# Optimization experiments

Hardware: AMD Instinct MI355X
Metric: run time of the kernel (lower is better)

## Reference

```python
import jax, jax.numpy as jnp
import numpy as np

B, T, F, H, OUT = 128, 512, 1, 512, 1


def setup_inputs() -> dict:
    key = jax.random.key(0)
    ks = jax.random.split(key, 12)
    s1 = 1.0 / np.sqrt(H)  # torch LSTMCell/Linear default init scale
    u = lambda k, shape, s: jax.random.uniform(k, shape, jnp.float32, -s, s)
    return {
        "x": jax.random.normal(ks[0], (B, T), jnp.float32),
        "W_ih1": u(ks[1], (4 * H, F), s1),
        "W_hh1": u(ks[2], (4 * H, H), s1),
        "b_ih1": u(ks[3], (4 * H,), s1),
        "b_hh1": u(ks[4], (4 * H,), s1),
        "W_ih2": u(ks[5], (4 * H, H), s1),
        "W_hh2": u(ks[6], (4 * H, H), s1),
        "b_ih2": u(ks[7], (4 * H,), s1),
        "b_hh2": u(ks[8], (4 * H,), s1),
        "W_out": u(ks[9], (OUT, H), s1),
        "b_out": u(ks[10], (OUT,), s1),
        "future": 32,
    }


def _lstm_cell(x_t, h, c, W_ih, W_hh, b_ih, b_hh):
    # gates: [B, 4H]; torch LSTMCell gate order: i, f, g, o
    gates = x_t @ W_ih.T + b_ih + h @ W_hh.T + b_hh
    i, f, g, o = jnp.split(gates, 4, axis=-1)
    c_new = jax.nn.sigmoid(f) * c + jax.nn.sigmoid(i) * jnp.tanh(g)
    h_new = jax.nn.sigmoid(o) * jnp.tanh(c_new)
    return h_new, c_new


def reference(x, W_ih1, W_hh1, b_ih1, b_hh1, W_ih2, W_hh2, b_ih2, b_hh2,
              W_out, b_out, future):
    bsz = x.shape[0]
    hid = W_hh1.shape[1]
    zeros = jnp.zeros((bsz, hid), x.dtype)

    def run_cells(x_t, h1, c1, h2, c2):
        h1, c1 = _lstm_cell(x_t, h1, c1, W_ih1, W_hh1, b_ih1, b_hh1)
        h2, c2 = _lstm_cell(h1, h2, c2, W_ih2, W_hh2, b_ih2, b_hh2)
        out = h2 @ W_out.T + b_out  # [B, 1]
        return h1, c1, h2, c2, out

    def step(carry, x_t):
        h1, c1, h2, c2 = carry
        h1, c1, h2, c2, out = run_cells(x_t, h1, c1, h2, c2)
        return (h1, c1, h2, c2), out

    xs = jnp.swapaxes(x, 0, 1)[..., None]  # [T, B, 1]
    carry, outs = jax.lax.scan(step, (zeros, zeros, zeros, zeros), xs)

    if future > 0:
        def fstep(carry, _):
            h1, c1, h2, c2, out = carry
            h1, c1, h2, c2, out = run_cells(out, h1, c1, h2, c2)
            return (h1, c1, h2, c2, out), out

        fcarry = (*carry, outs[-1])
        _, fouts = jax.lax.scan(fstep, fcarry, None, length=future)
        outs = jnp.concatenate([outs, fouts], axis=0)  # [T+future, B, 1]

    # stack(dim=1).squeeze(2) -> [B, T+future]
    return jnp.swapaxes(outs, 0, 1)[..., 0]
```

## Files before the change

kernel.cpp:

```cpp
#include <hip/hip_runtime.h>
#include <cstdint>

#define Hdim 512
#define Bdim 128
#define Tdim 512
#define FUT  32
#define TT   (Tdim + FUT)
#define NB1  64
#define NB2  128
#define NBO  2
#define NBLK (NB1 + NB2 + NBO)
#define RD   8
#define FSTR 32
#define F2B  64
#define FOB  200

typedef _Float16 f16;
typedef f16   half8 __attribute__((ext_vector_type(8)));
typedef float f32x4 __attribute__((ext_vector_type(4)));
typedef unsigned long long ull;

#define AW1_OFF 0
#define AW2_OFF (AW1_OFF + 1048576)
#define B1P_OFF (AW2_OFF + 2097152)
#define B2P_OFF (B1P_OFF + 2048)
#define WX1_OFF (B2P_OFF + 2048)
#define XT_OFF  (WX1_OFF + 2048)
#define H1P_OFF (XT_OFF + 65536)
#define H2P_OFF (H1P_OFF + 524288)
#define ARR_OFF (H2P_OFF + 524288)
#define WS_FLOATS (ARR_OFF + 8192)

__device__ __forceinline__ float sigm(float v) { return 1.0f / (1.0f + __expf(-v)); }
__device__ __forceinline__ float tanh_fast(float v) {
    v = fminf(fmaxf(v, -20.0f), 20.0f);
    float e = __expf(2.0f * v);
    return (e - 1.0f) / (e + 1.0f);
}

__device__ __forceinline__ unsigned cohloadu(const unsigned* p) {
    return __hip_atomic_load(p, __ATOMIC_RELAXED, __HIP_MEMORY_SCOPE_AGENT);
}
__device__ __forceinline__ ull cohload64(const ull* p) {
    return __hip_atomic_load(p, __ATOMIC_RELAXED, __HIP_MEMORY_SCOPE_AGENT);
}
__device__ __forceinline__ void cohstore64(ull* p, ull v) {
    __hip_atomic_store(p, v, __ATOMIC_RELAXED, __HIP_MEMORY_SCOPE_AGENT);
}

union HB { ull u[2]; half8 h; };
__device__ __forceinline__ half8 fragload(const half8* p) {
    const ull* q = (const ull*)p;
    HB t; t.u[0] = cohload64(q); t.u[1] = cohload64(q + 1);
    return t.h;
}

__global__ void lstm_prep(const float* __restrict__ x,
                          const float* __restrict__ W_ih1, const float* __restrict__ W_hh1,
                          const float* __restrict__ b_ih1, const float* __restrict__ b_hh1,
                          const float* __restrict__ W_ih2, const float* __restrict__ W_hh2,
                          const float* __restrict__ b_ih2, const float* __restrict__ b_hh2,
                          float* __restrict__ ws) {
    int i = blockIdx.x * blockDim.x + threadIdx.x;
    f16* aw1 = (f16*)(ws + AW1_OFF);
    f16* aw2 = (f16*)(ws + AW2_OFF);

    if (i < 131072) {
        int mt = i >> 10, rest = i & 1023, ks = rest >> 6, lane = rest & 63;
        int m = mt * 16 + (lane & 15);
        int u = m >> 2, g = m & 3;
        int kbase = ks * 32 + (lane >> 4) * 8;
        size_t ohi = ((((size_t)mt * 16 + ks) * 2 + 0) * 64 + lane) * 8;
        size_t olo = ((((size_t)mt * 16 + ks) * 2 + 1) * 64 + lane) * 8;
        #pragma unroll
        for (int j = 0; j < 8; ++j) {
            float wv = W_hh1[(size_t)(g * Hdim + u) * Hdim + kbase + j];
            f16 hi = (f16)wv;
            f16 lo = (f16)(wv - (float)hi);
            aw1[ohi + j] = hi; aw1[olo + j] = lo;
        }
    }
    if (i >= 131072 && i < 393216) {
        int i2 = i - 131072;
        int mt = i2 >> 11, rest = i2 & 2047, ks = rest >> 6, lane = rest & 63;
        int m = mt * 16 + (lane & 15);
        int u = m >> 2, g = m & 3;
        int kbase = ks * 32 + (lane >> 4) * 8;
        size_t ohi = ((((size_t)mt * 32 + ks) * 2 + 0) * 64 + lane) * 8;
        size_t olo = ((((size_t)mt * 32 + ks) * 2 + 1) * 64 + lane) * 8;
        #pragma unroll
        for (int j = 0; j < 8; ++j) {
            int k = kbase + j;
            float wv = (k < Hdim) ? W_ih2[(size_t)(g * Hdim + u) * Hdim + k]
                                  : W_hh2[(size_t)(g * Hdim + u) * Hdim + (k - Hdim)];
            f16 hi = (f16)wv;
            f16 lo = (f16)(wv - (float)hi);
            aw2[ohi + j] = hi; aw2[olo + j] = lo;
        }
    }
    if (i < Hdim) {
        float4 bb1 = { b_ih1[i] + b_hh1[i],               b_ih1[Hdim+i] + b_hh1[Hdim+i],
                       b_ih1[2*Hdim+i] + b_hh1[2*Hdim+i], b_ih1[3*Hdim+i] + b_hh1[3*Hdim+i] };
        float4 bb2 = { b_ih2[i] + b_hh2[i],               b_ih2[Hdim+i] + b_hh2[Hdim+i],
                       b_ih2[2*Hdim+i] + b_hh2[2*Hdim+i], b_ih2[3*Hdim+i] + b_hh2[3*Hdim+i] };
        float4 wx  = { W_ih1[i], W_ih1[Hdim+i], W_ih1[2*Hdim+i], W_ih1[3*Hdim+i] };
        ((float4*)(ws + B1P_OFF))[i] = bb1;
        ((float4*)(ws + B2P_OFF))[i] = bb2;
        ((float4*)(ws + WX1_OFF))[i] = wx;
    }
    if (i < Tdim * Bdim) {
        int t = i >> 7, b = i & 127;
        ws[XT_OFF + i] = x[b * Tdim + t];
    }
    if (i < 262144) {
        ((ull*)(ws + H1P_OFF))[i] = 0;
        ((ull*)(ws + H2P_OFF))[i] = 0;
    }
    if (i < 8192) ((unsigned*)(ws + ARR_OFF))[i] = 0u;
}

__global__ __launch_bounds__(256, 1) void lstm_main(float* ws,
                                                    const float* __restrict__ Wout,
                                                    const float* __restrict__ bout,
                                                    float* __restrict__ out) {
    const int tid  = threadIdx.x, bid = blockIdx.x;
    const int w    = tid >> 6;
    const int lane = tid & 63;
    const int quad = lane >> 4;
    const int col  = lane & 15;
    const bool is1  = (bid < NB1);
    const bool is2  = (bid >= NB1) && (bid < NB1 + NB2);
    const bool isout = (bid >= NB1 + NB2);

    __shared__ f16   awlds[65536];
    __shared__ float wout_lds[Hdim];
    __shared__ float psum[4][64];
    __shared__ float xflds[64];
    __shared__ float qpart[4][64];
    __shared__ ull   hstg[512];

    unsigned* flg = (unsigned*)(ws + ARR_OFF);
    unsigned short* stg = (unsigned short*)hstg;
    const float* xT = ws + XT_OFF;
    const float bout0 = bout[0];

    const int bid1 = is1 ? (bid & 31) : 0;
    const int gid  = is2 ? (bid - NB1) : 0;
    const int ug   = gid & 63;
    const int gA   = is1 ? (bid >> 5) : (is2 ? (gid >> 6) : (bid - NB1 - NB2));
    const int ntw  = gA * 4 + w;
    const int ks1  = bid1 >> 1, qp0 = (bid1 & 1) * 2;
    const int ks2  = ug >> 2,  qg  = ug & 3;

    auto wait3 = [&](unsigned T1, unsigned T2) {
        if (tid < 64) {
            for (;;) {
                unsigned v1 = (lane < 32) ? cohloadu(flg + (gA*32 + lane) * FSTR) : 0xFFFFFFFFu;
                unsigned v2 = cohloadu(flg + (F2B + gA*64 + lane) * FSTR);
                if (__all(v1 >= T1 && v2 >= T2)) break;
                __builtin_amdgcn_s_sleep(4);
            }
        }
        asm volatile("" ::: "memory");
        __syncthreads();
    };
    auto wait1o = [&](unsigned T1, unsigned To) {
        if (tid < 64) {
            for (;;) {
                unsigned v1 = (lane < 32) ? cohloadu(flg + (gA*32 + lane) * FSTR)  : 0xFFFFFFFFu;
                unsigned vo = (lane == 0) ? cohloadu(flg + (FOB + gA) * FSTR)      : 0xFFFFFFFFu;
                if (__all(v1 >= T1 && vo >= To)) break;
                __builtin_amdgcn_s_sleep(4);
            }
        }
        asm volatile("" ::: "memory");
        __syncthreads();
    };
    auto wait2f = [&](unsigned T2) {
        if (tid < 64) {
            for (;;) {
                unsigned v2 = cohloadu(flg + (F2B + gA*64 + lane) * FSTR);
                if (__all(v2 >= T2)) break;
                __builtin_amdgcn_s_sleep(4);
            }
        }
        asm volatile("" ::: "memory");
        __syncthreads();
    };
    auto post = [&](unsigned* slot, unsigned val) {
        __syncthreads();
        if (tid == 0)
            __hip_atomic_store(slot, val, __ATOMIC_RELAXED, __HIP_MEMORY_SCOPE_AGENT);
    };

    auto h1pf = [&](int par, int spl) {
        return (const half8*)((const unsigned short*)(ws + H1P_OFF) + (size_t)(par*2+spl) * 65536); };
    auto h2pf = [&](int par, int spl) {
        return (const half8*)((const unsigned short*)(ws + H2P_OFF) + (size_t)(par*2+spl) * 65536); };
    auto h1ull = [&](int par, int spl) {
        return (ull*)(ws + H1P_OFF) + (size_t)(par*2+spl) * 16384; };
    auto h2ull = [&](int par, int spl) {
        return (ull*)(ws + H2P_OFF) + (size_t)(par*2+spl) * 16384; };

    if (is1) {
        half8* d = (half8*)awlds;
        const half8* s = (const half8*)(ws + AW1_OFF) + (size_t)bid1 * 8192;
        for (int i = tid; i < 8192; i += 256) d[i] = s[i];
    } else if (is2) {
        half8* d = (half8*)awlds;
        const half8* s = (const half8*)(ws + AW2_OFF) + (size_t)ug * 8192;
        for (int i = tid; i < 8192; i += 256) d[i] = s[i];
    }
    wout_lds[tid]       = Wout[tid];
    wout_lds[256 + tid] = Wout[256 + tid];
    __syncthreads();
    const half8* aw8 = (const half8*)awlds;

    const int bcol = ntw * 16 + col;
    int   u_[4];  float4 b1v[4], wxv[4];  float c1s[4];
    int   u2_[2]; float4 b2v[2];          float c2s[2];
    if (is1) {
        #pragma unroll
        for (int mt = 0; mt < 4; ++mt) {
            u_[mt]  = bid1 * 16 + mt * 4 + quad;
            b1v[mt] = ((const float4*)(ws + B1P_OFF))[u_[mt]];
            wxv[mt] = ((const float4*)(ws + WX1_OFF))[u_[mt]];
            c1s[mt] = 0.0f;
        }
    } else if (is2) {
        #pragma unroll
        for (int mt = 0; mt < 2; ++mt) {
            u2_[mt] = ug * 8 + mt * 4 + quad;
            b2v[mt] = ((const float4*)(ws + B2P_OFF))[u2_[mt]];
            c2s[mt] = 0.0f;
        }
    }

    auto stage1 = [&](int mt, float hv) {
        f16 hhi = (f16)hv;
        f16 hlo = (f16)(hv - (float)hhi);
        int mq = mt*4 + quad, qp = mq >> 3, jj = mq & 7;
        int hi = ((w*2 + qp)*16 + col)*8 + jj;
        stg[hi]        = __builtin_bit_cast(unsigned short, hhi);
        stg[1024 + hi] = __builtin_bit_cast(unsigned short, hlo);
    };
    auto store1 = [&](int dpar) {
        __syncthreads();
        #pragma unroll
        for (int k = 0; k < 2; ++k) {
            int f = k * 256 + tid;
            int spl = f >> 8, r = f & 255;
            int ntl = r >> 6, rr = r & 63;
            int qp = rr >> 5, r2 = rr & 31, colp = r2 >> 1, pos = r2 & 1;
            cohstore64(h1ull(dpar, spl)
                       + (((gA*4 + ntl)*16 + ks1)*64 + (qp0 + qp)*16 + colp)*2 + pos,
                       hstg[f]);
        }
    };

    auto gemm1 = [&](int spar, int dpar, float xv) {
        f32x4 acc[4] = {};
        const half8* fh = h1pf(spar, 0);
        const half8* fl = h1pf(spar, 1);
        half8 rh[8], rl[8];
        #pragma unroll
        for (int ks = 0; ks < 8; ++ks) {
            rh[ks] = fragload(fh + (ntw*16+ks)*64 + lane);
            rl[ks] = fragload(fl + (ntw*16+ks)*64 + lane);
        }
        #pragma unroll
        for (int ks = 0; ks < 16; ++ks) {
            half8 b0h = rh[ks&7], b0l = rl[ks&7];
            if (ks < 8) {
                int kp = ks + 8;
                rh[ks&7] = fragload(fh + (ntw*16+kp)*64 + lane);
                rl[ks&7] = fragload(fl + (ntw*16+kp)*64 + lane);
            }
            #pragma unroll
            for (int mt = 0; mt < 4; ++mt) {
                half8 ah = aw8[((mt*16 + ks)*2 + 0)*64 + lane];
                half8 al = aw8[((mt*16 + ks)*2 + 1)*64 + lane];
                acc[mt] = __builtin_amdgcn_mfma_f32_16x16x32_f16(ah, b0h, acc[mt], 0, 0, 0);
                acc[mt] = __builtin_amdgcn_mfma_f32_16x16x32_f16(al, b0h, acc[mt], 0, 0, 0);
                acc[mt] = __builtin_amdgcn_mfma_f32_16x16x32_f16(ah, b0l, acc[mt], 0, 0, 0);
            }
        }
        #pragma unroll
        for (int mt = 0; mt < 4; ++mt) {
            f32x4 g = acc[mt];
            float pi = g[0] + b1v[mt].x + wxv[mt].x * xv;
            float pf = g[1] + b1v[mt].y + wxv[mt].y * xv;
            float pg = g[2] + b1v[mt].z + wxv[mt].z * xv;
            float po = g[3] + b1v[mt].w + wxv[mt].w * xv;
            float c = fmaf(sigm(pf), c1s[mt], sigm(pi) * tanh_fast(pg));
            c1s[mt] = c;
            stage1(mt, sigm(po) * tanh_fast(c));
        }
        store1(dpar);
    };

    auto g2_step = [&](int s) {
        int cpar = s & 7, ppar = (s - 1) & 7;
        const half8* fh = h1pf(cpar, 0);
        const half8* fl = h1pf(cpar, 1);
        const half8* gh = h2pf(ppar, 0);
        const half8* gl = h2pf(ppar, 1);

        wait1o((unsigned)(s + 1), (s >= RD) ? (unsigned)(s - (RD - 1)) : 0u);
        half8 rh[8], rl[8];
        #pragma unroll
        for (int ks = 0; ks < 8; ++ks) {
            rh[ks] = fragload(fh + (ntw*16+ks)*64 + lane);
            rl[ks] = fragload(fl + (ntw*16+ks)*64 + lane);
        }
        wait2f((unsigned)s);

        f32x4 acc[2] = {};
        #pragma unroll
        for (int ks = 0; ks < 32; ++ks) {
            half8 b0h = rh[ks&7], b0l = rl[ks&7];
            if (ks < 24) {
                int kp = ks + 8;
                const half8* sh = (kp < 16) ? fh : gh;
                const half8* sl = (kp < 16) ? fl : gl;
                int kq = (kp < 16) ? kp : kp - 16;
                rh[ks&7] = fragload(sh + (ntw*16+kq)*64 + lane);
                rl[ks&7] = fragload(sl + (ntw*16+kq)*64 + lane);
            }
            #pragma unroll
            for (int mt = 0; mt < 2; ++mt) {
                half8 ah = aw8[((mt*32 + ks)*2 + 0)*64 + lane];
                half8 al = aw8[((mt*32 + ks)*2 + 1)*64 + lane];
                acc[mt] = __builtin_amdgcn_mfma_f32_16x16x32_f16(ah, b0h, acc[mt], 0, 0, 0);
                acc[mt] = __builtin_amdgcn_mfma_f32_16x16x32_f16(al, b0h, acc[mt], 0, 0, 0);
                acc[mt] = __builtin_amdgcn_mfma_f32_16x16x32_f16(ah, b0l, acc[mt], 0, 0, 0);
            }
        }
        #pragma unroll
        for (int mt = 0; mt < 2; ++mt) {
            f32x4 g = acc[mt];
            float pi = g[0] + b2v[mt].x;
            float pf = g[1] + b2v[mt].y;
            float pg = g[2] + b2v[mt].z;
            float po = g[3] + b2v[mt].w;
            float c = fmaf(sigm(pf), c2s[mt], sigm(pi) * tanh_fast(pg));
            c2s[mt] = c;
            float hv = sigm(po) * tanh_fast(c);
            f16 hhi = (f16)hv;
            f16 hlo = (f16)(hv - (float)hhi);
            int idx = ((w*16 + col)*8 + (mt*4 + quad));
            stg[idx]       = __builtin_bit_cast(unsigned short, hhi);
            stg[512 + idx] = __builtin_bit_cast(unsigned short, hlo);
        }
        __syncthreads();
        {
            int f = tid;
            int spl = f >> 7, r = f & 127;
            int ntl = r >> 5, colp = (r >> 1) & 15, pos = r & 1;
            int nt = gA * 4 + ntl;
            cohstore64(h2ull(cpar, spl) + ((nt*16 + ks2)*64 + qg*16 + colp)*2 + pos, hstg[f]);
        }
        post(&flg[(F2B + gA*64 + ug) * FSTR], (unsigned)(s + 1));
    };

    if (is1) {
        #pragma unroll
        for (int mt = 0; mt < 4; ++mt) {
            float xv = xT[bcol];
            float pi = b1v[mt].x + wxv[mt].x * xv;
            float pg = b1v[mt].z + wxv[mt].z * xv;
            float po = b1v[mt].w + wxv[mt].w * xv;
            float c = sigm(pi) * tanh_fast(pg);
            c1s[mt] = c;
            stage1(mt, sigm(po) * tanh_fast(c));
        }
        store1(0);
        post(&flg[(gA*32 + bid1) * FSTR], 1u);

        for (int t = 0; t <= Tdim - 2; ++t) {
            wait3((unsigned)(t + 1), (t >= RD - 1) ? (unsigned)(t - (RD - 2)) : 0u);
            gemm1(t & 7, (t + 1) & 7, xT[(t + 1) * Bdim + bcol]);
            post(&flg[(gA*32 + bid1) * FSTR], (unsigned)(t + 2));
        }

        for (int t = Tdim; t < TT; ++t) {
            wait3((unsigned)t, (unsigned)t);
            {
                int bl = tid & 63, kh = tid >> 6;
                int nt = gA * 4 + (bl >> 4), nl = bl & 15;
                const half8* ph = h2pf((t - 1) & 7, 0);
                const half8* pl = h2pf((t - 1) & 7, 1);
                float a = 0.0f;
                #pragma unroll
                for (int kk = 0; kk < 4; ++kk) {
                    int ks = kh * 4 + kk;
                    #pragma unroll
                    for (int qd = 0; qd < 4; ++qd) {
                        half8 vh = fragload(ph + (nt*16+ks)*64 + qd*16 + nl);
                        half8 vl = fragload(pl + (nt*16+ks)*64 + qd*16 + nl);
                        int ub = ks*32 + qd*8;
                        #pragma unroll
                        for (int j = 0; j < 8; ++j)
                            a = fmaf((float)vh[j] + (float)vl[j], wout_lds[ub + j], a);
                    }
                }
                psum[kh][bl] = a;
                __syncthreads();
                if (tid < 64)
                    xflds[tid] = psum[0][tid] + psum[1][tid] + psum[2][tid]
                               + psum[3][tid] + bout0;
                __syncthreads();
                if (bid1 == 0 && tid < 64 && (t - 1) >= Tdim)
                    out[(size_t)(gA*64 + tid) * TT + (t - 1)] = xflds[tid];
            }
            gemm1((t - 1) & 7, t & 7, xflds[bcol & 63]);
            post(&flg[(gA*32 + bid1) * FSTR], (unsigned)(t + 1));
        }
    }
    else if (is2) {
        for (int s = 0; s < TT; ++s) g2_step(s);
    }
    else {
        int b = gA * 64 + lane;
        int nt = b >> 4, nl = b & 15;
        for (int s = 0; s < TT; ++s) {
            wait2f((unsigned)(s + 1));
            const half8* ph = h2pf(s & 7, 0);
            const half8* pl = h2pf(s & 7, 1);
            float a = 0.0f;
            #pragma unroll
            for (int kk = 0; kk < 4; ++kk) {
                int ks = w * 4 + kk;
                #pragma unroll
                for (int qd = 0; qd < 4; ++qd) {
                    half8 vh = fragload(ph + (nt*16+ks)*64 + qd*16 + nl);
                    half8 vl = fragload(pl + (nt*16+ks)*64 + qd*16 + nl);
                    int ub = ks*32 + qd*8;
                    #pragma unroll
                    for (int j = 0; j < 8; ++j)
                        a = fmaf((float)vh[j] + (float)vl[j], wout_lds[ub + j], a);
                }
            }
            qpart[w][lane] = a;
            __syncthreads();
            if (w == 0)
                out[(size_t)b * TT + s] = qpart[0][lane] + qpart[1][lane]
                                        + qpart[2][lane] + qpart[3][lane] + bout0;
            post(&flg[(FOB + gA) * FSTR], (unsigned)(s + 1));
        }
    }
}

extern "C" void kernel_launch(void* const* d_in, const int* in_sizes, int n_in,
                              void* d_out, int out_size, void* d_ws, size_t ws_size,
                              hipStream_t stream) {
    const float* x     = (const float*)d_in[0];
    const float* W_ih1 = (const float*)d_in[1];
    const float* W_hh1 = (const float*)d_in[2];
    const float* b_ih1 = (const float*)d_in[3];
    const float* b_hh1 = (const float*)d_in[4];
    const float* W_ih2 = (const float*)d_in[5];
    const float* W_hh2 = (const float*)d_in[6];
    const float* b_ih2 = (const float*)d_in[7];
    const float* b_hh2 = (const float*)d_in[8];
    const float* W_out = (const float*)d_in[9];
    const float* b_out = (const float*)d_in[10];
    float* ws  = (float*)d_ws;
    float* out = (float*)d_out;

    hipLaunchKernelGGL(lstm_prep, dim3(1536), dim3(256), 0, stream,
                       x, W_ih1, W_hh1, b_ih1, b_hh1, W_ih2, W_hh2, b_ih2, b_hh2, ws);
    hipLaunchKernelGGL(lstm_main, dim3(NBLK), dim3(256), 0, stream,
                       ws, W_out, b_out, out);
}
```

Before: 3.886 ms.

## Assign LSTM roles per XCD and split layer-2 input projection into separate pipeline

Blocks now read their XCC ID, take an ordinal through an atomic counter, and pick a role from which XCD they run on, so each layer's 32 cooperating blocks share one XCD's L2 for flag and hidden-state exchange. Layer 2's concatenated [W_ih2|W_hh2] GEMM is split into two stages. A new group of blocks computes the W_ih2·h1 + bias projection into a double-buffered partial buffer, and the recurrent blocks only do the W_hh2·h2 half. That shortens the serial critical path and pipelines it one step behind layer 1. Output reduction is split across four blocks per group with atomicAdd, and spin-waits get an iteration cap. The risk is that the role mapping assumes blocks spread evenly over XCDs; if they do not, the cap can leave the output wrong.

```diff
diff --git a/kernel.cpp b/kernel.cpp
--- a/kernel.cpp
+++ b/kernel.cpp
@@ -6,30 +6,33 @@
 #define Tdim 512
 #define FUT  32
 #define TT   (Tdim + FUT)
-#define NB1  64
-#define NB2  128
-#define NBO  2
-#define NBLK (NB1 + NB2 + NBO)
 #define RD   8
 #define FSTR 32
-#define F2B  64
-#define FOB  200
+#define CAPIT (1 << 22)
 
 typedef _Float16 f16;
-typedef f16   half8 __attribute__((ext_vector_type(8)));
-typedef float f32x4 __attribute__((ext_vector_type(4)));
+typedef f16      half8  __attribute__((ext_vector_type(8)));
+typedef float    f32x4  __attribute__((ext_vector_type(4)));
 typedef unsigned long long ull;
 
-#define AW1_OFF 0
-#define AW2_OFF (AW1_OFF + 1048576)
-#define B1P_OFF (AW2_OFF + 2097152)
-#define B2P_OFF (B1P_OFF + 2048)
-#define WX1_OFF (B2P_OFF + 2048)
-#define XT_OFF  (WX1_OFF + 2048)
-#define H1P_OFF (XT_OFF + 65536)
-#define H2P_OFF (H1P_OFF + 524288)
-#define ARR_OFF (H2P_OFF + 524288)
+#define AW1_OFF  0
+#define AW2R_OFF (AW1_OFF + 1048576)
+#define AW2I_OFF (AW2R_OFF + 1048576)
+#define B1P_OFF  (AW2I_OFF + 1048576)
+#define B2P_OFF  (B1P_OFF + 2048)
+#define WX1_OFF  (B2P_OFF + 2048)
+#define XT_OFF   (WX1_OFF + 2048)
+#define H1G_OFF  (XT_OFF + 65536)
+#define H2G_OFF  (H1G_OFF + 524288)
+#define H1L0_OFF (H2G_OFF + 524288)
+#define PB_OFF   (H1L0_OFF + 1048576)
+#define ARR_OFF  (PB_OFF + 524288)
 #define WS_FLOATS (ARR_OFF + 8192)
+
+#define F1Gp(g,i)  (flg + ((g)*32 + (i)) * FSTR)
+#define FPp(g,i)   (flg + (64 + (g)*32 + (i)) * FSTR)
+#define F2Gp(g,i)  (flg + (128 + (g)*32 + (i)) * FSTR)
+#define FOGp(g,q)  (flg + (192 + (g)*4 + (q)) * FSTR)
 
 __device__ __forceinline__ float sigm(float v) { return 1.0f / (1.0f + __expf(-v)); }
 __device__ __forceinline__ float tanh_fast(float v) {
@@ -41,14 +44,17 @@
 __device__ __forceinline__ unsigned cohloadu(const unsigned* p) {
     return __hip_atomic_load(p, __ATOMIC_RELAXED, __HIP_MEMORY_SCOPE_AGENT);
 }
+__device__ __forceinline__ void cohstoreu(unsigned* p, unsigned v) {
+    __hip_atomic_store(p, v, __ATOMIC_RELAXED, __HIP_MEMORY_SCOPE_AGENT);
+}
 __device__ __forceinline__ ull cohload64(const ull* p) {
     return __hip_atomic_load(p, __ATOMIC_RELAXED, __HIP_MEMORY_SCOPE_AGENT);
 }
 __device__ __forceinline__ void cohstore64(ull* p, ull v) {
     __hip_atomic_store(p, v, __ATOMIC_RELAXED, __HIP_MEMORY_SCOPE_AGENT);
 }
-
-union HB { ull u[2]; half8 h; };
+union HB  { ull u[2]; half8 h; };
+union HB4 { ull u[2]; f32x4 f; };
 __device__ __forceinline__ half8 fragload(const half8* p) {
     const ull* q = (const ull*)p;
     HB t; t.u[0] = cohload64(q); t.u[1] = cohload64(q + 1);
@@ -60,10 +66,11 @@
                           const float* __restrict__ b_ih1, const float* __restrict__ b_hh1,
                           const float* __restrict__ W_ih2, const float* __restrict__ W_hh2,
                           const float* __restrict__ b_ih2, const float* __restrict__ b_hh2,
-                          float* __restrict__ ws) {
+                          float* __restrict__ ws, float* __restrict__ out) {
     int i = blockIdx.x * blockDim.x + threadIdx.x;
-    f16* aw1 = (f16*)(ws + AW1_OFF);
-    f16* aw2 = (f16*)(ws + AW2_OFF);
+    f16* aw1  = (f16*)(ws + AW1_OFF);
+    f16* aw2r = (f16*)(ws + AW2R_OFF);
+    f16* aw2i = (f16*)(ws + AW2I_OFF);
 
     if (i < 131072) {
         int mt = i >> 10, rest = i & 1023, ks = rest >> 6, lane = rest & 63;
@@ -80,22 +87,36 @@
             aw1[ohi + j] = hi; aw1[olo + j] = lo;
         }
     }
-    if (i >= 131072 && i < 393216) {
+    if (i >= 131072 && i < 262144) {
         int i2 = i - 131072;
-        int mt = i2 >> 11, rest = i2 & 2047, ks = rest >> 6, lane = rest & 63;
+        int mt = i2 >> 10, rest = i2 & 1023, ks = rest >> 6, lane = rest & 63;
         int m = mt * 16 + (lane & 15);
         int u = m >> 2, g = m & 3;
         int kbase = ks * 32 + (lane >> 4) * 8;
-        size_t ohi = ((((size_t)mt * 32 + ks) * 2 + 0) * 64 + lane) * 8;
-        size_t olo = ((((size_t)mt * 32 + ks) * 2 + 1) * 64 + lane) * 8;
+        size_t ohi = ((((size_t)mt * 16 + ks) * 2 + 0) * 64 + lane) * 8;
+        size_t olo = ((((size_t)mt * 16 + ks) * 2 + 1) * 64 + lane) * 8;
         #pragma unroll
         for (int j = 0; j < 8; ++j) {
-            int k = kbase + j;
-            float wv = (k < Hdim) ? W_ih2[(size_t)(g * Hdim + u) * Hdim + k]
-                                  : W_hh2[(size_t)(g * Hdim + u) * Hdim + (k - Hdim)];
+            float wv = W_hh2[(size_t)(g * Hdim + u) * Hdim + kbase + j];
             f16 hi = (f16)wv;
             f16 lo = (f16)(wv - (float)hi);
-            aw2[ohi + j] = hi; aw2[olo + j] = lo;
+            aw2r[ohi + j] = hi; aw2r[olo + j] = lo;
+        }
+    }
+    if (i >= 262144 && i < 393216) {
+        int i2 = i - 262144;
+        int mt = i2 >> 10, rest = i2 & 1023, ks = rest >> 6, lane = rest & 63;
+        int m = mt * 16 + (lane & 15);
+        int u = m >> 2, g = m & 3;
+        int kbase = ks * 32 + (lane >> 4) * 8;
+        size_t ohi = ((((size_t)mt * 16 + ks) * 2 + 0) * 64 + lane) * 8;
+        size_t olo = ((((size_t)mt * 16 + ks) * 2 + 1) * 64 + lane) * 8;
+        #pragma unroll
+        for (int j = 0; j < 8; ++j) {
+            float wv = W_ih2[(size_t)(g * Hdim + u) * Hdim + kbase + j];
+            f16 hi = (f16)wv;
+            f16 lo = (f16)(wv - (float)hi);
+            aw2i[ohi + j] = hi; aw2i[olo + j] = lo;
         }
     }
     if (i < Hdim) {
@@ -113,292 +134,221 @@
         ws[XT_OFF + i] = x[b * Tdim + t];
     }
     if (i < 262144) {
-        ((ull*)(ws + H1P_OFF))[i] = 0;
-        ((ull*)(ws + H2P_OFF))[i] = 0;
+        ((ull*)(ws + H1G_OFF))[i] = 0;
+        ((ull*)(ws + H2G_OFF))[i] = 0;
+        ((ull*)(ws + H1L0_OFF))[i] = 0;
+        ((ull*)(ws + PB_OFF))[i & 262143] = 0;
     }
     if (i < 8192) ((unsigned*)(ws + ARR_OFF))[i] = 0u;
+    if (i < Bdim * TT) out[i] = 0.f;
 }
 
 __global__ __launch_bounds__(256, 1) void lstm_main(float* ws,
                                                     const float* __restrict__ Wout,
                                                     const float* __restrict__ bout,
                                                     float* __restrict__ out) {
-    const int tid  = threadIdx.x, bid = blockIdx.x;
+    const int tid  = threadIdx.x;
     const int w    = tid >> 6;
     const int lane = tid & 63;
     const int quad = lane >> 4;
     const int col  = lane & 15;
-    const bool is1  = (bid < NB1);
-    const bool is2  = (bid >= NB1) && (bid < NB1 + NB2);
-    const bool isout = (bid >= NB1 + NB2);
 
     __shared__ f16   awlds[65536];
     __shared__ float wout_lds[Hdim];
     __shared__ float psum[4][64];
     __shared__ float xflds[64];
     __shared__ float qpart[4][64];
-    __shared__ ull   hstg[512];
+    __shared__ __align__(16) ull hstg[512];
+    __shared__ int sXcd, sOrd, badf;
 
     unsigned* flg = (unsigned*)(ws + ARR_OFF);
     unsigned short* stg = (unsigned short*)hstg;
     const float* xT = ws + XT_OFF;
     const float bout0 = bout[0];
 
-    const int bid1 = is1 ? (bid & 31) : 0;
-    const int gid  = is2 ? (bid - NB1) : 0;
-    const int ug   = gid & 63;
-    const int gA   = is1 ? (bid >> 5) : (is2 ? (gid >> 6) : (bid - NB1 - NB2));
-    const int ntw  = gA * 4 + w;
-    const int ks1  = bid1 >> 1, qp0 = (bid1 & 1) * 2;
-    const int ks2  = ug >> 2,  qg  = ug & 3;
-
-    auto wait3 = [&](unsigned T1, unsigned T2) {
-        if (tid < 64) {
-            for (;;) {
-                unsigned v1 = (lane < 32) ? cohloadu(flg + (gA*32 + lane) * FSTR) : 0xFFFFFFFFu;
-                unsigned v2 = cohloadu(flg + (F2B + gA*64 + lane) * FSTR);
-                if (__all(v1 >= T1 && v2 >= T2)) break;
-                __builtin_amdgcn_s_sleep(4);
-            }
-        }
-        asm volatile("" ::: "memory");
-        __syncthreads();
+    if (tid == 0) {
+        badf = 0;
+        unsigned xcc;
+        asm volatile("s_getreg_b32 %0, hwreg(HW_REG_XCC_ID, 0, 32)" : "=s"(xcc));
+        xcc &= 0xF;
+        sXcd = (int)xcc;
+        sOrd = (int)atomicAdd(flg + (200 + xcc) * FSTR, 1u);
+    }
+    __syncthreads();
+    const int xcd = sXcd, ord = sOrd;
+
+    const bool is1   = (xcd < 2);
+    const bool is2   = (xcd == 2 || xcd == 3);
+    const bool isI   = (xcd == 4 || xcd == 5);
+    const bool isout = (xcd == 6) && (ord < 8);
+    const bool active = ((is1 || is2 || isI) && ord < 32) || isout;
+    if (!active) return;
+
+    const int gA  = is1 ? xcd : is2 ? (xcd - 2) : isI ? (xcd - 4) : (ord >> 2);
+    const int oq  = isout ? (ord & 3) : 0;
+    const int ntw = gA * 4 + w;
+    const int ks1 = ord >> 1, qp0 = (ord & 1) * 2;
+
+    auto h1pf = [&](int par, int spl) {
+        return (const half8*)((const unsigned short*)(ws + H1G_OFF) + (size_t)(par*2+spl) * 65536); };
+    auto h2pf = [&](int par, int spl) {
+        return (const half8*)((const unsigned short*)(ws + H2G_OFF) + (size_t)(par*2+spl) * 65536); };
+    auto h1ull = [&](int par, int spl) {
+        return (ull*)(ws + H1G_OFF) + (size_t)(par*2+spl) * 16384; };
+    auto h2ull = [&](int par, int spl) {
+        return (ull*)(ws + H2G_OFF) + (size_t)(par*2+spl) * 16384; };
+    auto pidx = [&](int par2, int mt) -> size_t {
+        return ((((size_t)par2 * 2 + gA) * 32 + ord) * 16 + (mt * 4 + w)) * 64 + lane;
     };
-    auto wait1o = [&](unsigned T1, unsigned To) {
-        if (tid < 64) {
-            for (;;) {
-                unsigned v1 = (lane < 32) ? cohloadu(flg + (gA*32 + lane) * FSTR)  : 0xFFFFFFFFu;
-                unsigned vo = (lane == 0) ? cohloadu(flg + (FOB + gA) * FSTR)      : 0xFFFFFFFFu;
-                if (__all(v1 >= T1 && vo >= To)) break;
-                __builtin_amdgcn_s_sleep(4);
-            }
-        }
-        asm volatile("" ::: "memory");
-        __syncthreads();
-    };
-    auto wait2f = [&](unsigned T2) {
-        if (tid < 64) {
-            for (;;) {
-                unsigned v2 = cohloadu(flg + (F2B + gA*64 + lane) * FSTR);
-                if (__all(v2 >= T2)) break;
-                __builtin_amdgcn_s_sleep(4);
-            }
-        }
-        asm volatile("" ::: "memory");
-        __syncthreads();
-    };
-    auto post = [&](unsigned* slot, unsigned val) {
-        __syncthreads();
-        if (tid == 0)
-            __hip_atomic_store(slot, val, __ATOMIC_RELAXED, __HIP_MEMORY_SCOPE_AGENT);
-    };
-
-    auto h1pf = [&](int par, int spl) {
-        return (const half8*)((const unsigned short*)(ws + H1P_OFF) + (size_t)(par*2+spl) * 65536); };
-    auto h2pf = [&](int par, int spl) {
-        return (const half8*)((const unsigned short*)(ws + H2P_OFF) + (size_t)(par*2+spl) * 65536); };
-    auto h1ull = [&](int par, int spl) {
-        return (ull*)(ws + H1P_OFF) + (size_t)(par*2+spl) * 16384; };
-    auto h2ull = [&](int par, int spl) {
-        return (ull*)(ws + H2P_OFF) + (size_t)(par*2+spl) * 16384; };
-
-    if (is1) {
+    ull* Pu = (ull*)(ws + PB_OFF);
+
+    if (is1 || is2 || isI) {
+        const half8* s = (const half8*)(ws + (is1 ? AW1_OFF : is2 ? AW2R_OFF : AW2I_OFF))
+                       + (size_t)ord * 8192;
         half8* d = (half8*)awlds;
-        const half8* s = (const half8*)(ws + AW1_OFF) + (size_t)bid1 * 8192;
-        for (int i = tid; i < 8192; i += 256) d[i] = s[i];
-    } else if (is2) {
-        half8* d = (half8*)awlds;
-        const half8* s = (const half8*)(ws + AW2_OFF) + (size_t)ug * 8192;
         for (int i = tid; i < 8192; i += 256) d[i] = s[i];
     }
     wout_lds[tid]       = Wout[tid];
     wout_lds[256 + tid] = Wout[256 + tid];
     __syncthreads();
-    const half8* aw8 = (const half8*)awlds;
-
-    const int bcol = ntw * 16 + col;
-    int   u_[4];  float4 b1v[4], wxv[4];  float c1s[4];
-    int   u2_[2]; float4 b2v[2];          float c2s[2];
-    if (is1) {
-        #pragma unroll
-        for (int mt = 0; mt < 4; ++mt) {
-            u_[mt]  = bid1 * 16 + mt * 4 + quad;
-            b1v[mt] = ((const float4*)(ws + B1P_OFF))[u_[mt]];
-            wxv[mt] = ((const float4*)(ws + WX1_OFF))[u_[mt]];
-            c1s[mt] = 0.0f;
-        }
-    } else if (is2) {
-        #pragma unroll
-        for (int mt = 0; mt < 2; ++mt) {
-            u2_[mt] = ug * 8 + mt * 4 + quad;
-            b2v[mt] = ((const float4*)(ws + B2P_OFF))[u2_[mt]];
-            c2s[mt] = 0.0f;
-        }
-    }
+
+    auto gemm = [&](const half8* fh, const half8* fl, f32x4* acc) {
+        half8 rh[16], rl[16];
+        #pragma unroll
+        for (int ks = 0; ks < 16; ++ks) {
+            rh[ks] = fragload(fh + (ntw * 16 + ks) * 64 + lane);
+            rl[ks] = fragload(fl + (ntw * 16 + ks) * 64 + lane);
+        }
+        const half8* aw8 = (const half8*)awlds;
+        #pragma unroll
+        for (int ks = 0; ks < 16; ++ks) {
+            #pragma unroll
+            for (int mt = 0; mt < 4; ++mt) {
+                half8 ah = aw8[((mt * 16 + ks) * 2 + 0) * 64 + lane];
+                half8 al = aw8[((mt * 16 + ks) * 2 + 1) * 64 + lane];
+                acc[mt] = __builtin_amdgcn_mfma_f32_16x16x32_f16(ah, rh[ks], acc[mt], 0, 0, 0);
+                acc[mt] = __builtin_amdgcn_mfma_f32_16x16x32_f16(al, rh[ks], acc[mt], 0, 0, 0);
+                acc[mt] = __builtin_amdgcn_mfma_f32_16x16x32_f16(ah, rl[ks], acc[mt], 0, 0, 0);
+            }
+        }
+    };
 
     auto stage1 = [&](int mt, float hv) {
         f16 hhi = (f16)hv;
         f16 hlo = (f16)(hv - (float)hhi);
-        int mq = mt*4 + quad, qp = mq >> 3, jj = mq & 7;
-        int hi = ((w*2 + qp)*16 + col)*8 + jj;
+        int mq = mt * 4 + quad, qp = mq >> 3, jj = mq & 7;
+        int hi = ((w * 2 + qp) * 16 + col) * 8 + jj;
         stg[hi]        = __builtin_bit_cast(unsigned short, hhi);
         stg[1024 + hi] = __builtin_bit_cast(unsigned short, hlo);
     };
-    auto store1 = [&](int dpar) {
+    auto publish = [&](int dpar, bool to1) {
         __syncthreads();
-        #pragma unroll
-        for (int k = 0; k < 2; ++k) {
-            int f = k * 256 + tid;
-            int spl = f >> 8, r = f & 255;
-            int ntl = r >> 6, rr = r & 63;
-            int qp = rr >> 5, r2 = rr & 31, colp = r2 >> 1, pos = r2 & 1;
-            cohstore64(h1ull(dpar, spl)
-                       + (((gA*4 + ntl)*16 + ks1)*64 + (qp0 + qp)*16 + colp)*2 + pos,
-                       hstg[f]);
-        }
+        int f = 2 * tid;
+        int spl = f >> 8, rmix = f & 255, ntl = rmix >> 6, rr = rmix & 63;
+        int qp = rr >> 5, colp = (rr & 31) >> 1;
+        size_t e = (((size_t)(gA * 4 + ntl) * 16 + ks1) * 64 + (qp0 + qp) * 16 + colp) * 2;
+        ull* base = (to1 ? h1ull(dpar, spl) : h2ull(dpar, spl)) + e;
+        cohstore64(base,     hstg[f]);
+        cohstore64(base + 1, hstg[f + 1]);
     };
 
-    auto gemm1 = [&](int spar, int dpar, float xv) {
-        f32x4 acc[4] = {};
-        const half8* fh = h1pf(spar, 0);
-        const half8* fl = h1pf(spar, 1);
-        half8 rh[8], rl[8];
-        #pragma unroll
-        for (int ks = 0; ks < 8; ++ks) {
-            rh[ks] = fragload(fh + (ntw*16+ks)*64 + lane);
-            rl[ks] = fragload(fl + (ntw*16+ks)*64 + lane);
-        }
-        #pragma unroll
-        for (int ks = 0; ks < 16; ++ks) {
-            half8 b0h = rh[ks&7], b0l = rl[ks&7];
-            if (ks < 8) {
-                int kp = ks + 8;
-                rh[ks&7] = fragload(fh + (ntw*16+kp)*64 + lane);
-                rl[ks&7] = fragload(fl + (ntw*16+kp)*64 + lane);
-            }
+    if (is1) {
+        const int bcol = ntw * 16 + col;
+        float4 b1v[4], wxv[4]; float c1s[4];
+        #pragma unroll
+        for (int mt = 0; mt < 4; ++mt) {
+            int u = ord * 16 + mt * 4 + quad;
+            b1v[mt] = ((const float4*)(ws + B1P_OFF))[u];
+            wxv[mt] = ((const float4*)(ws + WX1_OFF))[u];
+            c1s[mt] = 0.f;
+        }
+        unsigned* myF1 = F1Gp(gA, ord);
+        unsigned fPc = (tid < 64 && lane >= 32) ? 0u : 0xFFFFFFFFu;
+
+        auto wait_main = [&](unsigned T1, unsigned TP) {
+            if (tid < 64 && !badf) {
+                int gd = 0;
+                for (;;) {
+                    unsigned a = (lane < 32) ? cohloadu(F1Gp(gA, lane)) : 0xFFFFFFFFu;
+                    if (lane >= 32 && fPc < TP) fPc = cohloadu(FPp(gA, lane - 32));
+                    if (__all(a >= T1 && fPc >= TP)) break;
+                    if (++gd > CAPIT) { badf = 1; break; }
+                    __builtin_amdgcn_s_sleep(4);
+                }
+            }
+            asm volatile("" ::: "memory");
+            __syncthreads();
+        };
+        auto wait_fut = [&](unsigned T) {
+            if (tid < 64 && !badf) {
+                int gd = 0;
+                for (;;) {
+                    unsigned a = (lane < 32) ? cohloadu(F1Gp(gA, lane))
+                                             : cohloadu(F2Gp(gA, lane - 32));
+                    if (__all(a >= T)) break;
+                    if (++gd > CAPIT) { badf = 1; break; }
+                    __builtin_amdgcn_s_sleep(4);
+                }
+            }
+            asm volatile("" ::: "memory");
+            __syncthreads();
+        };
+        auto post1 = [&](unsigned v) {
+            __syncthreads();
+            if (tid == 0) cohstoreu(myF1, v);
+        };
+        auto l1_step = [&](int spar, int dpar, float xv) {
+            f32x4 acc[4] = {};
+            gemm(h1pf(spar, 0), h1pf(spar, 1), acc);
             #pragma unroll
             for (int mt = 0; mt < 4; ++mt) {
-                half8 ah = aw8[((mt*16 + ks)*2 + 0)*64 + lane];
-                half8 al = aw8[((mt*16 + ks)*2 + 1)*64 + lane];
-                acc[mt] = __builtin_amdgcn_mfma_f32_16x16x32_f16(ah, b0h, acc[mt], 0, 0, 0);
-                acc[mt] = __builtin_amdgcn_mfma_f32_16x16x32_f16(al, b0h, acc[mt], 0, 0, 0);
-                acc[mt] = __builtin_amdgcn_mfma_f32_16x16x32_f16(ah, b0l, acc[mt], 0, 0, 0);
-            }
-        }
-        #pragma unroll
-        for (int mt = 0; mt < 4; ++mt) {
-            f32x4 g = acc[mt];
-            float pi = g[0] + b1v[mt].x + wxv[mt].x * xv;
-            float pf = g[1] + b1v[mt].y + wxv[mt].y * xv;
-            float pg = g[2] + b1v[mt].z + wxv[mt].z * xv;
-            float po = g[3] + b1v[mt].w + wxv[mt].w * xv;
-            float c = fmaf(sigm(pf), c1s[mt], sigm(pi) * tanh_fast(pg));
-            c1s[mt] = c;
-            stage1(mt, sigm(po) * tanh_fast(c));
-        }
-        store1(dpar);
-    };
-
-    auto g2_step = [&](int s) {
-        int cpar = s & 7, ppar = (s - 1) & 7;
-        const half8* fh = h1pf(cpar, 0);
-        const half8* fl = h1pf(cpar, 1);
-        const half8* gh = h2pf(ppar, 0);
-        const half8* gl = h2pf(ppar, 1);
-
-        wait1o((unsigned)(s + 1), (s >= RD) ? (unsigned)(s - (RD - 1)) : 0u);
-        half8 rh[8], rl[8];
-        #pragma unroll
-        for (int ks = 0; ks < 8; ++ks) {
-            rh[ks] = fragload(fh + (ntw*16+ks)*64 + lane);
-            rl[ks] = fragload(fl + (ntw*16+ks)*64 + lane);
-        }
-        wait2f((unsigned)s);
-
-        f32x4 acc[2] = {};
-        #pragma unroll
-        for (int ks = 0; ks < 32; ++ks) {
-            half8 b0h = rh[ks&7], b0l = rl[ks&7];
-            if (ks < 24) {
-                int kp = ks + 8;
-                const half8* sh = (kp < 16) ? fh : gh;
-                const half8* sl = (kp < 16) ? fl : gl;
-                int kq = (kp < 16) ? kp : kp - 16;
-                rh[ks&7] = fragload(sh + (ntw*16+kq)*64 + lane);
-                rl[ks&7] = fragload(sl + (ntw*16+kq)*64 + lane);
-            }
-            #pragma unroll
-            for (int mt = 0; mt < 2; ++mt) {
-                half8 ah = aw8[((mt*32 + ks)*2 + 0)*64 + lane];
-                half8 al = aw8[((mt*32 + ks)*2 + 1)*64 + lane];
-                acc[mt] = __builtin_amdgcn_mfma_f32_16x16x32_f16(ah, b0h, acc[mt], 0, 0, 0);
-                acc[mt] = __builtin_amdgcn_mfma_f32_16x16x32_f16(al, b0h, acc[mt], 0, 0, 0);
-                acc[mt] = __builtin_amdgcn_mfma_f32_16x16x32_f16(ah, b0l, acc[mt], 0, 0, 0);
-            }
-        }
-        #pragma unroll
-        for (int mt = 0; mt < 2; ++mt) {
-            f32x4 g = acc[mt];
-            float pi = g[0] + b2v[mt].x;
-            float pf = g[1] + b2v[mt].y;
-            float pg = g[2] + b2v[mt].z;
-            float po = g[3] + b2v[mt].w;
-            float c = fmaf(sigm(pf), c2s[mt], sigm(pi) * tanh_fast(pg));
-            c2s[mt] = c;
-            float hv = sigm(po) * tanh_fast(c);
-            f16 hhi = (f16)hv;
-            f16 hlo = (f16)(hv - (float)hhi);
-            int idx = ((w*16 + col)*8 + (mt*4 + quad));
-            stg[idx]       = __builtin_bit_cast(unsigned short, hhi);
-            stg[512 + idx] = __builtin_bit_cast(unsigned short, hlo);
-        }
-        __syncthreads();
+                f32x4 g = acc[mt];
+                float pi = g[0] + b1v[mt].x + wxv[mt].x * xv;
+                float pf = g[1] + b1v[mt].y + wxv[mt].y * xv;
+                float pg = g[2] + b1v[mt].z + wxv[mt].z * xv;
+                float po = g[3] + b1v[mt].w + wxv[mt].w * xv;
+                float c = fmaf(sigm(pf), c1s[mt], sigm(pi) * tanh_fast(pg));
+                c1s[mt] = c;
+                stage1(mt, sigm(po) * tanh_fast(c));
+            }
+            publish(dpar, true);
+        };
+
         {
-            int f = tid;
-            int spl = f >> 7, r = f & 127;
-            int ntl = r >> 5, colp = (r >> 1) & 15, pos = r & 1;
-            int nt = gA * 4 + ntl;
-            cohstore64(h2ull(cpar, spl) + ((nt*16 + ks2)*64 + qg*16 + colp)*2 + pos, hstg[f]);
-        }
-        post(&flg[(F2B + gA*64 + ug) * FSTR], (unsigned)(s + 1));
-    };
-
-    if (is1) {
-        #pragma unroll
-        for (int mt = 0; mt < 4; ++mt) {
             float xv = xT[bcol];
-            float pi = b1v[mt].x + wxv[mt].x * xv;
-            float pg = b1v[mt].z + wxv[mt].z * xv;
-            float po = b1v[mt].w + wxv[mt].w * xv;
-            float c = sigm(pi) * tanh_fast(pg);
-            c1s[mt] = c;
-            stage1(mt, sigm(po) * tanh_fast(c));
-        }
-        store1(0);
-        post(&flg[(gA*32 + bid1) * FSTR], 1u);
-
+            #pragma unroll
+            for (int mt = 0; mt < 4; ++mt) {
+                float pi = b1v[mt].x + wxv[mt].x * xv;
+                float pg = b1v[mt].z + wxv[mt].z * xv;
+                float po = b1v[mt].w + wxv[mt].w * xv;
+                float c = sigm(pi) * tanh_fast(pg);
+                c1s[mt] = c;
+                stage1(mt, sigm(po) * tanh_fast(c));
+            }
+            publish(0, true);
+            post1(1u);
+        }
         for (int t = 0; t <= Tdim - 2; ++t) {
-            wait3((unsigned)(t + 1), (t >= RD - 1) ? (unsigned)(t - (RD - 2)) : 0u);
-            gemm1(t & 7, (t + 1) & 7, xT[(t + 1) * Bdim + bcol]);
-            post(&flg[(gA*32 + bid1) * FSTR], (unsigned)(t + 2));
-        }
-
+            wait_main((unsigned)(t + 1), (t >= 7) ? (unsigned)(t - 6) : 0u);
+            l1_step(t & 7, (t + 1) & 7, xT[(t + 1) * Bdim + bcol]);
+            post1((unsigned)(t + 2));
+        }
         for (int t = Tdim; t < TT; ++t) {
-            wait3((unsigned)t, (unsigned)t);
+            wait_fut((unsigned)t);
             {
                 int bl = tid & 63, kh = tid >> 6;
-                int nt = gA * 4 + (bl >> 4), nl = bl & 15;
+                int nt2 = gA * 4 + (bl >> 4), nl = bl & 15;
                 const half8* ph = h2pf((t - 1) & 7, 0);
                 const half8* pl = h2pf((t - 1) & 7, 1);
-                float a = 0.0f;
+                float a = 0.f;
                 #pragma unroll
                 for (int kk = 0; kk < 4; ++kk) {
                     int ks = kh * 4 + kk;
                     #pragma unroll
                     for (int qd = 0; qd < 4; ++qd) {
-                        half8 vh = fragload(ph + (nt*16+ks)*64 + qd*16 + nl);
-                        half8 vl = fragload(pl + (nt*16+ks)*64 + qd*16 + nl);
-                        int ub = ks*32 + qd*8;
+                        half8 vh = fragload(ph + (nt2 * 16 + ks) * 64 + qd * 16 + nl);
+                        half8 vl = fragload(pl + (nt2 * 16 + ks) * 64 + qd * 16 + nl);
+                        int ub = ks * 32 + qd * 8;
                         #pragma unroll
                         for (int j = 0; j < 8; ++j)
                             a = fmaf((float)vh[j] + (float)vl[j], wout_lds[ub + j], a);
@@ -410,43 +360,160 @@
                     xflds[tid] = psum[0][tid] + psum[1][tid] + psum[2][tid]
                                + psum[3][tid] + bout0;
                 __syncthreads();
-                if (bid1 == 0 && tid < 64 && (t - 1) >= Tdim)
-                    out[(size_t)(gA*64 + tid) * TT + (t - 1)] = xflds[tid];
-            }
-            gemm1((t - 1) & 7, t & 7, xflds[bcol & 63]);
-            post(&flg[(gA*32 + bid1) * FSTR], (unsigned)(t + 1));
+            }
+            l1_step((t - 1) & 7, t & 7, xflds[bcol & 63]);
+            post1((unsigned)(t + 1));
         }
     }
     else if (is2) {
-        for (int s = 0; s < TT; ++s) g2_step(s);
+        float c2s[4] = {0.f, 0.f, 0.f, 0.f};
+        unsigned* myF2 = F2Gp(gA, ord);
+        unsigned* myFP = FPp(gA, ord);
+        unsigned fPc2 = (tid < 64 && lane == 0) ? 0u : 0xFFFFFFFFu;
+        unsigned fogc = (tid < 64 && lane >= 32 && lane < 36) ? 0u : 0xFFFFFFFFu;
+
+        auto waitP = [&](unsigned T) {
+            if (tid < 64 && !badf) {
+                int gd = 0;
+                for (;;) {
+                    if (lane == 0 && fPc2 < T) fPc2 = cohloadu(myFP);
+                    if (__all(fPc2 >= T)) break;
+                    if (++gd > CAPIT) { badf = 1; break; }
+                    __builtin_amdgcn_s_sleep(4);
+                }
+            }
+            asm volatile("" ::: "memory");
+            __syncthreads();
+        };
+        auto waitB = [&](unsigned T2, unsigned To) {
+            if (tid < 64 && !badf) {
+                int gd = 0;
+                for (;;) {
+                    unsigned a = (lane < 32) ? cohloadu(F2Gp(gA, lane)) : 0xFFFFFFFFu;
+                    if (lane >= 32 && lane < 36 && fogc < To) fogc = cohloadu(FOGp(gA, lane - 32));
+                    if (__all(a >= T2 && fogc >= To)) break;
+                    if (++gd > CAPIT) { badf = 1; break; }
+                    __builtin_amdgcn_s_sleep(4);
+                }
+            }
+            asm volatile("" ::: "memory");
+            __syncthreads();
+        };
+
+        for (int s = 0; s < TT; ++s) {
+            int cpar = s & 7, ppar = (s - 1) & 7;
+            waitP((unsigned)(s + 1));
+            HB4 praw[4];
+            #pragma unroll
+            for (int mt = 0; mt < 4; ++mt) {
+                const ull* q = Pu + pidx(s & 1, mt) * 2;
+                praw[mt].u[0] = cohload64(q);
+                praw[mt].u[1] = cohload64(q + 1);
+            }
+            waitB((unsigned)s, (s >= 8) ? (unsigned)(s - 7) : 0u);
+
+            f32x4 acc[4] = {};
+            if (s > 0) gemm(h2pf(ppar, 0), h2pf(ppar, 1), acc);
+            #pragma unroll
+            for (int mt = 0; mt < 4; ++mt) {
+                f32x4 g = acc[mt];
+                f32x4 p = praw[mt].f;
+                float pi = g[0] + p[0], pf = g[1] + p[1];
+                float pg = g[2] + p[2], po = g[3] + p[3];
+                float c = fmaf(sigm(pf), c2s[mt], sigm(pi) * tanh_fast(pg));
+                c2s[mt] = c;
+                stage1(mt, sigm(po) * tanh_fast(c));
+            }
+            publish(cpar, false);
+            __syncthreads();
+            if (tid == 0) cohstoreu(myF2, (unsigned)(s + 1));
+        }
+    }
+    else if (isI) {
+        float4 b2v[4];
+        #pragma unroll
+        for (int mt = 0; mt < 4; ++mt)
+            b2v[mt] = ((const float4*)(ws + B2P_OFF))[ord * 16 + mt * 4 + quad];
+        unsigned* myFP = FPp(gA, ord);
+        unsigned f1c = (tid < 64 && lane < 32) ? 0u : 0xFFFFFFFFu;
+        unsigned f2c = (tid < 64 && lane >= 32) ? 0u : 0xFFFFFFFFu;
+
+        auto waitI = [&](unsigned T1, unsigned T2) {
+            if (tid < 64 && !badf) {
+                int gd = 0;
+                for (;;) {
+                    if (lane < 32 && f1c < T1) f1c = cohloadu(F1Gp(gA, lane));
+                    if (lane >= 32 && f2c < T2) f2c = cohloadu(F2Gp(gA, lane - 32));
+                    if (__all(f1c >= T1 && f2c >= T2)) break;
+                    if (++gd > CAPIT) { badf = 1; break; }
+                    __builtin_amdgcn_s_sleep(4);
+                }
+            }
+            asm volatile("" ::: "memory");
+            __syncthreads();
+        };
+
+        for (int s = 0; s < TT; ++s) {
+            waitI((unsigned)(s + 1), (s >= 2) ? (unsigned)(s - 1) : 0u);
+            f32x4 acc[4] = {};
+            gemm(h1pf(s & 7, 0), h1pf(s & 7, 1), acc);
+            #pragma unroll
+            for (int mt = 0; mt < 4; ++mt) {
+                HB4 p;
+                p.f = acc[mt];
+                p.f[0] += b2v[mt].x; p.f[1] += b2v[mt].y;
+                p.f[2] += b2v[mt].z; p.f[3] += b2v[mt].w;
+                ull* q = Pu + pidx(s & 1, mt) * 2;
+                cohstore64(q,     p.u[0]);
+                cohstore64(q + 1, p.u[1]);
+            }
+            __syncthreads();
+            if (tid == 0) cohstoreu(myFP, (unsigned)(s + 1));
+        }
     }
     else {
         int b = gA * 64 + lane;
         int nt = b >> 4, nl = b & 15;
+        int ks = oq * 4 + w;
+        unsigned* myFO = FOGp(gA, oq);
+
+        auto waitO = [&](unsigned T) {
+            if (tid < 64 && !badf) {
+                int gd = 0;
+                for (;;) {
+                    unsigned a = (lane < 32) ? cohloadu(F2Gp(gA, lane)) : 0xFFFFFFFFu;
+                    if (__all(a >= T)) break;
+                    if (++gd > CAPIT) { badf = 1; break; }
+                    __builtin_amdgcn_s_sleep(4);
+                }
+            }
+            asm volatile("" ::: "memory");
+            __syncthreads();
+        };
+
         for (int s = 0; s < TT; ++s) {
-            wait2f((unsigned)(s + 1));
+            waitO((unsigned)(s + 1));
             const half8* ph = h2pf(s & 7, 0);
             const half8* pl = h2pf(s & 7, 1);
-            float a = 0.0f;
-            #pragma unroll
-            for (int kk = 0; kk < 4; ++kk) {
-                int ks = w * 4 + kk;
+            float a = 0.f;
+            #pragma unroll
+            for (int qd = 0; qd < 4; ++qd) {
+                half8 vh = fragload(ph + (nt * 16 + ks) * 64 + qd * 16 + nl);
+                half8 vl = fragload(pl + (nt * 16 + ks) * 64 + qd * 16 + nl);
+                int ub = ks * 32 + qd * 8;
                 #pragma unroll
-                for (int qd = 0; qd < 4; ++qd) {
-                    half8 vh = fragload(ph + (nt*16+ks)*64 + qd*16 + nl);
-                    half8 vl = fragload(pl + (nt*16+ks)*64 + qd*16 + nl);
-                    int ub = ks*32 + qd*8;
-                    #pragma unroll
-                    for (int j = 0; j < 8; ++j)
-                        a = fmaf((float)vh[j] + (float)vl[j], wout_lds[ub + j], a);
-                }
+                for (int j = 0; j < 8; ++j)
+                    a = fmaf((float)vh[j] + (float)vl[j], wout_lds[ub + j], a);
             }
             qpart[w][lane] = a;
             __syncthreads();
-            if (w == 0)
-                out[(size_t)b * TT + s] = qpart[0][lane] + qpart[1][lane]
-                                        + qpart[2][lane] + qpart[3][lane] + bout0;
-            post(&flg[(FOB + gA) * FSTR], (unsigned)(s + 1));
+            if (w == 0) {
+                float v = qpart[0][lane] + qpart[1][lane] + qpart[2][lane] + qpart[3][lane];
+                if (oq == 0) v += bout0;
+                atomicAdd(&out[(size_t)b * TT + s], v);
+            }
+            __syncthreads();
+            if (tid == 0) cohstoreu(myFO, (unsigned)(s + 1));
         }
     }
 }
@@ -469,7 +536,7 @@
     float* out = (float*)d_out;
 
     hipLaunchKernelGGL(lstm_prep, dim3(1536), dim3(256), 0, stream,
-                       x, W_ih1, W_hh1, b_ih1, b_hh1, W_ih2, W_hh2, b_ih2, b_hh2, ws);
-    hipLaunchKernelGGL(lstm_main, dim3(NBLK), dim3(256), 0, stream,
+                       x, W_ih1, W_hh1, b_ih1, b_hh1, W_ih2, W_hh2, b_ih2, b_hh2, ws, out);
+    hipLaunchKernelGGL(lstm_main, dim3(256), dim3(256), 0, stream,
                        ws, W_out, b_out, out);
 }
```

New measurement: 4.553 ms. 1.17x slower.
